# Kernel optimization log

Measured on AMD Instinct MI355X. Metric: run time of the kernel, lower is better.

The kernel has to match this reference:

```python
import jax, jax.numpy as jnp
import numpy as np
from jax import lax

MIN_VALUE = 0.0
MAX_VALUE = 1.0

# 5-point Laplacian stencil kernel, OIHW layout
_LAP_KERNEL = jnp.array([[0.0, 1.0, 0.0],
                         [1.0, -4.0, 1.0],
                         [0.0, 1.0, 0.0]], dtype=jnp.float32).reshape(1, 1, 3, 3)


def _laplacian(u):
    # u: [B, 1, H, W], zero-padded 3x3 stencil (SAME)
    return lax.conv_general_dilated(
        u, _LAP_KERNEL, window_strides=(1, 1), padding='SAME',
        dimension_numbers=('NCHW', 'OIHW', 'NCHW'))


def _step(u, params):
    # Fisher-Kolmogorov reaction-diffusion step:
    #   diff = D * laplacian(u) + rho * u * (1 - u)
    D = params[:, 0:1]    # [B,1,H,W]
    rho = params[:, 1:2]  # [B,1,H,W]
    return D * _laplacian(u) + rho * u * (1.0 - u)


def setup_inputs() -> dict:
    key = jax.random.key(0)
    k1, k2, k3 = jax.random.split(key, 3)
    B, H, W = 32, 256, 256
    u = jax.random.uniform(k1, (B, 1, H, W), dtype=jnp.float32)
    params = jax.random.uniform(k2, (B, 2, H, W), dtype=jnp.float32)
    t = jax.random.randint(k3, (B,), 0, 32, dtype=jnp.int32)
    return {"u": u, "params": params, "t": t}


def reference(u, params, t):
    # Original: for step in range(max(t)): u[t>step] += step(u[t>step], params[t>step]); clip(u).
    # The step is per-sample local, so masked gather/scatter == predicated full update.
    max_duration = int(jnp.max(t))  # static trip count

    def body(step, u):
        mask = (t > step).astype(u.dtype)[:, None, None, None]  # [B,1,1,1]
        u = u + mask * _step(u, params)
        return jnp.clip(u, MIN_VALUE, MAX_VALUE)

    return lax.fori_loop(0, max_duration, body, u)
```

## Files before the change

### kernel.cpp

```cpp
#include <hip/hip_runtime.h>

#define HH 256
#define WW 256
#define PLANE (HH * WW)
#define CORE 32
#define HALO 8
#define SLAB 48
#define NW 16
#define RPW 3

__global__ __launch_bounds__(1024, 4)
void rd_group_kernel(const float* __restrict__ uin,
                     const float* __restrict__ params,
                     const int* __restrict__ t,
                     float* __restrict__ uout,
                     int base, int k)
{
    __shared__ float4 vt[NW][64];
    __shared__ float4 vb[NW][64];

    const int blk   = blockIdx.x;
    const int b     = blk >> 3;
    const int strip = blk & 7;
    const int r0    = strip * CORE;
    const int w     = threadIdx.x >> 6;
    const int lane  = threadIdx.x & 63;
    const int c0    = lane << 2;

    const int growbase = r0 - HALO + RPW * w;

    int ls = t[b] - base;
    ls = ls < 0 ? 0 : (ls > k ? k : ls);

    float u[RPW][4], pD[RPW][4], pR[RPW][4];
    bool inimg[RPW];

    const size_t ubase = (size_t)b * PLANE;
    const size_t pbase = (size_t)b * 2 * PLANE;

    #pragma unroll
    for (int dr = 0; dr < RPW; ++dr) {
        const int grow = growbase + dr;
        inimg[dr] = (grow >= 0) && (grow < HH);
        if (inimg[dr]) {
            const float4 uu = *reinterpret_cast<const float4*>(uin + ubase + (size_t)grow * WW + c0);
            const float4 dd = *reinterpret_cast<const float4*>(params + pbase + (size_t)grow * WW + c0);
            const float4 rr = *reinterpret_cast<const float4*>(params + pbase + PLANE + (size_t)grow * WW + c0);
            u[dr][0] = uu.x; u[dr][1] = uu.y; u[dr][2] = uu.z; u[dr][3] = uu.w;
            pD[dr][0] = dd.x; pD[dr][1] = dd.y; pD[dr][2] = dd.z; pD[dr][3] = dd.w;
            pR[dr][0] = rr.x; pR[dr][1] = rr.y; pR[dr][2] = rr.z; pR[dr][3] = rr.w;
        } else {
            #pragma unroll
            for (int c = 0; c < 4; ++c) { u[dr][c] = 0.f; pD[dr][c] = 0.f; pR[dr][c] = 0.f; }
        }
    }

    for (int s = 0; s < ls; ++s) {
        vt[w][lane] = make_float4(u[0][0], u[0][1], u[0][2], u[0][3]);
        vb[w][lane] = make_float4(u[RPW-1][0], u[RPW-1][1], u[RPW-1][2], u[RPW-1][3]);
        __syncthreads();

        float upr[4] = {0.f, 0.f, 0.f, 0.f};
        float dnr[4] = {0.f, 0.f, 0.f, 0.f};
        if (w > 0)      { float4 v = vb[w-1][lane]; upr[0]=v.x; upr[1]=v.y; upr[2]=v.z; upr[3]=v.w; }
        if (w < NW - 1) { float4 v = vt[w+1][lane]; dnr[0]=v.x; dnr[1]=v.y; dnr[2]=v.z; dnr[3]=v.w; }

        float nu[RPW][4];
        #pragma unroll
        for (int dr = 0; dr < RPW; ++dr) {
            float lf = __shfl_up(u[dr][3], 1);
            if (lane == 0)  lf = 0.f;
            float rt = __shfl_down(u[dr][0], 1);
            if (lane == 63) rt = 0.f;

            #pragma unroll
            for (int c = 0; c < 4; ++c) {
                const float upv = dr ? u[dr-1][c] : upr[c];
                const float dnv = (dr < RPW - 1) ? u[dr+1][c] : dnr[c];
                const float lv  = c ? u[dr][c-1] : lf;
                const float rv  = (c < 3) ? u[dr][c+1] : rt;
                const float uc  = u[dr][c];
                const float lap = upv + dnv + lv + rv - 4.0f * uc;
                float un = uc + pD[dr][c] * lap + pR[dr][c] * (uc * (1.0f - uc));
                un = fminf(fmaxf(un, 0.0f), 1.0f);
                nu[dr][c] = un;
            }
        }
        #pragma unroll
        for (int dr = 0; dr < RPW; ++dr) {
            #pragma unroll
            for (int c = 0; c < 4; ++c)
                u[dr][c] = inimg[dr] ? nu[dr][c] : 0.f;
        }
        __syncthreads();
    }

    #pragma unroll
    for (int dr = 0; dr < RPW; ++dr) {
        const int grow = growbase + dr;
        if (grow >= r0 && grow < r0 + CORE) {
            *reinterpret_cast<float4*>(uout + ubase + (size_t)grow * WW + c0) =
                make_float4(u[dr][0], u[dr][1], u[dr][2], u[dr][3]);
        }
    }
}

extern "C" void kernel_launch(void* const* d_in, const int* in_sizes, int n_in,
                              void* d_out, int out_size, void* d_ws, size_t ws_size,
                              hipStream_t stream) {
    (void)in_sizes; (void)n_in; (void)out_size; (void)ws_size;
    const float* u      = (const float*)d_in[0];
    const float* params = (const float*)d_in[1];
    const int*   t      = (const int*)d_in[2];
    float*       out    = (float*)d_out;
    float*       ws     = (float*)d_ws;

    const dim3 grid(256), block(1024);
    rd_group_kernel<<<grid, block, 0, stream>>>(u,   params, t, ws,  0,  8);
    rd_group_kernel<<<grid, block, 0, stream>>>(ws,  params, t, out, 8,  8);
    rd_group_kernel<<<grid, block, 0, stream>>>(out, params, t, ws,  16, 8);
    rd_group_kernel<<<grid, block, 0, stream>>>(ws,  params, t, out, 24, 7);
}
```

Measured before the change: 60.06 us.

## Deepen temporal blocking to 16 steps per launch with double-buffered halo exchange

Widens the halo from 8 to 16 rows with 4 rows per wave, which halves the number of launches from four to two. Each launch therefore re-reads u and params from global memory half as often. Shared-memory halo buffers are now double-buffered, which removes one __syncthreads per step. Rows that cannot influence the core within the remaining steps skip their loads, and the per-step clamp to zero outside the image is dropped in favour of zero params. The cost is more redundant halo compute (64 rows computed per 32 stored) and more registers per thread.

```diff
diff --git a/kernel.cpp b/kernel.cpp
--- a/kernel.cpp
+++ b/kernel.cpp
@@ -4,20 +4,20 @@
 #define WW 256
 #define PLANE (HH * WW)
 #define CORE 32
-#define HALO 8
-#define SLAB 48
+#define HALO 16
+#define SLAB 64
 #define NW 16
-#define RPW 3
+#define RPW 4
 
 __global__ __launch_bounds__(1024, 4)
-void rd_group_kernel(const float* __restrict__ uin,
-                     const float* __restrict__ params,
-                     const int* __restrict__ t,
-                     float* __restrict__ uout,
-                     int base, int k)
+void rd_tb16_kernel(const float* __restrict__ uin,
+                    const float* __restrict__ params,
+                    const int* __restrict__ t,
+                    float* __restrict__ uout,
+                    int base, int k)
 {
-    __shared__ float4 vt[NW][64];
-    __shared__ float4 vb[NW][64];
+    __shared__ float4 vt[2][NW][64];
+    __shared__ float4 vb[2][NW][64];
 
     const int blk   = blockIdx.x;
     const int b     = blk >> 3;
@@ -27,78 +27,91 @@
     const int lane  = threadIdx.x & 63;
     const int c0    = lane << 2;
 
-    const int growbase = r0 - HALO + RPW * w;
-
     int ls = t[b] - base;
     ls = ls < 0 ? 0 : (ls > k ? k : ls);
 
-    float u[RPW][4], pD[RPW][4], pR[RPW][4];
-    bool inimg[RPW];
-
+    const int growbase = r0 - HALO + RPW * w;
     const size_t ubase = (size_t)b * PLANE;
     const size_t pbase = (size_t)b * 2 * PLANE;
+
+    float u[RPW][4], pD[RPW][4], pR[RPW][4];
 
     #pragma unroll
     for (int dr = 0; dr < RPW; ++dr) {
         const int grow = growbase + dr;
-        inimg[dr] = (grow >= 0) && (grow < HH);
-        if (inimg[dr]) {
+        const bool inimg = (grow >= 0) && (grow < HH);
+        int dist = 0;
+        if (grow < r0)             dist = r0 - grow;
+        else if (grow > r0 + CORE - 1) dist = grow - (r0 + CORE - 1);
+        const bool needU = inimg && (dist <= ls);
+        const bool needP = inimg && (dist < ls);
+
+        if (needU) {
             const float4 uu = *reinterpret_cast<const float4*>(uin + ubase + (size_t)grow * WW + c0);
+            u[dr][0] = uu.x; u[dr][1] = uu.y; u[dr][2] = uu.z; u[dr][3] = uu.w;
+        } else {
+            u[dr][0] = u[dr][1] = u[dr][2] = u[dr][3] = 0.f;
+        }
+        if (needP) {
             const float4 dd = *reinterpret_cast<const float4*>(params + pbase + (size_t)grow * WW + c0);
             const float4 rr = *reinterpret_cast<const float4*>(params + pbase + PLANE + (size_t)grow * WW + c0);
-            u[dr][0] = uu.x; u[dr][1] = uu.y; u[dr][2] = uu.z; u[dr][3] = uu.w;
             pD[dr][0] = dd.x; pD[dr][1] = dd.y; pD[dr][2] = dd.z; pD[dr][3] = dd.w;
             pR[dr][0] = rr.x; pR[dr][1] = rr.y; pR[dr][2] = rr.z; pR[dr][3] = rr.w;
         } else {
-            #pragma unroll
-            for (int c = 0; c < 4; ++c) { u[dr][c] = 0.f; pD[dr][c] = 0.f; pR[dr][c] = 0.f; }
+            pD[dr][0] = pD[dr][1] = pD[dr][2] = pD[dr][3] = 0.f;
+            pR[dr][0] = pR[dr][1] = pR[dr][2] = pR[dr][3] = 0.f;
         }
     }
 
-    for (int s = 0; s < ls; ++s) {
-        vt[w][lane] = make_float4(u[0][0], u[0][1], u[0][2], u[0][3]);
-        vb[w][lane] = make_float4(u[RPW-1][0], u[RPW-1][1], u[RPW-1][2], u[RPW-1][3]);
-        __syncthreads();
+    if (ls > 0) {
+        vt[0][w][lane] = make_float4(u[0][0], u[0][1], u[0][2], u[0][3]);
+        vb[0][w][lane] = make_float4(u[RPW-1][0], u[RPW-1][1], u[RPW-1][2], u[RPW-1][3]);
 
-        float upr[4] = {0.f, 0.f, 0.f, 0.f};
-        float dnr[4] = {0.f, 0.f, 0.f, 0.f};
-        if (w > 0)      { float4 v = vb[w-1][lane]; upr[0]=v.x; upr[1]=v.y; upr[2]=v.z; upr[3]=v.w; }
-        if (w < NW - 1) { float4 v = vt[w+1][lane]; dnr[0]=v.x; dnr[1]=v.y; dnr[2]=v.z; dnr[3]=v.w; }
+        for (int s = 0; s < ls; ++s) {
+            __syncthreads();
+            const int cur = s & 1;
 
-        float nu[RPW][4];
+            float upr[4] = {0.f, 0.f, 0.f, 0.f};
+            float dnr[4] = {0.f, 0.f, 0.f, 0.f};
+            if (w > 0)      { float4 v = vb[cur][w-1][lane]; upr[0]=v.x; upr[1]=v.y; upr[2]=v.z; upr[3]=v.w; }
+            if (w < NW - 1) { float4 v = vt[cur][w+1][lane]; dnr[0]=v.x; dnr[1]=v.y; dnr[2]=v.z; dnr[3]=v.w; }
+
+            float nu[RPW][4];
+            #pragma unroll
+            for (int dr = 0; dr < RPW; ++dr) {
+                float lf = __shfl_up(u[dr][3], 1);
+                if (lane == 0)  lf = 0.f;
+                float rt = __shfl_down(u[dr][0], 1);
+                if (lane == 63) rt = 0.f;
+
+                #pragma unroll
+                for (int c = 0; c < 4; ++c) {
+                    const float upv = dr ? u[dr-1][c] : upr[c];
+                    const float dnv = (dr < RPW - 1) ? u[dr+1][c] : dnr[c];
+                    const float lv  = c ? u[dr][c-1] : lf;
+                    const float rv  = (c < 3) ? u[dr][c+1] : rt;
+                    const float uc  = u[dr][c];
+                    const float lap = upv + dnv + lv + rv - 4.0f * uc;
+                    float un = uc + pD[dr][c] * lap + pR[dr][c] * (uc * (1.0f - uc));
+                    nu[dr][c] = fminf(fmaxf(un, 0.0f), 1.0f);
+                }
+            }
+            #pragma unroll
+            for (int dr = 0; dr < RPW; ++dr)
+                #pragma unroll
+                for (int c = 0; c < 4; ++c)
+                    u[dr][c] = nu[dr][c];
+
+            const int nxt = cur ^ 1;
+            vt[nxt][w][lane] = make_float4(u[0][0], u[0][1], u[0][2], u[0][3]);
+            vb[nxt][w][lane] = make_float4(u[RPW-1][0], u[RPW-1][1], u[RPW-1][2], u[RPW-1][3]);
+        }
+    }
+
+    if (w >= HALO / RPW && w < (HALO + CORE) / RPW) {
         #pragma unroll
         for (int dr = 0; dr < RPW; ++dr) {
-            float lf = __shfl_up(u[dr][3], 1);
-            if (lane == 0)  lf = 0.f;
-            float rt = __shfl_down(u[dr][0], 1);
-            if (lane == 63) rt = 0.f;
-
-            #pragma unroll
-            for (int c = 0; c < 4; ++c) {
-                const float upv = dr ? u[dr-1][c] : upr[c];
-                const float dnv = (dr < RPW - 1) ? u[dr+1][c] : dnr[c];
-                const float lv  = c ? u[dr][c-1] : lf;
-                const float rv  = (c < 3) ? u[dr][c+1] : rt;
-                const float uc  = u[dr][c];
-                const float lap = upv + dnv + lv + rv - 4.0f * uc;
-                float un = uc + pD[dr][c] * lap + pR[dr][c] * (uc * (1.0f - uc));
-                un = fminf(fmaxf(un, 0.0f), 1.0f);
-                nu[dr][c] = un;
-            }
-        }
-        #pragma unroll
-        for (int dr = 0; dr < RPW; ++dr) {
-            #pragma unroll
-            for (int c = 0; c < 4; ++c)
-                u[dr][c] = inimg[dr] ? nu[dr][c] : 0.f;
-        }
-        __syncthreads();
-    }
-
-    #pragma unroll
-    for (int dr = 0; dr < RPW; ++dr) {
-        const int grow = growbase + dr;
-        if (grow >= r0 && grow < r0 + CORE) {
+            const int grow = growbase + dr;
             *reinterpret_cast<float4*>(uout + ubase + (size_t)grow * WW + c0) =
                 make_float4(u[dr][0], u[dr][1], u[dr][2], u[dr][3]);
         }
@@ -116,8 +129,6 @@
     float*       ws     = (float*)d_ws;
 
     const dim3 grid(256), block(1024);
-    rd_group_kernel<<<grid, block, 0, stream>>>(u,   params, t, ws,  0,  8);
-    rd_group_kernel<<<grid, block, 0, stream>>>(ws,  params, t, out, 8,  8);
-    rd_group_kernel<<<grid, block, 0, stream>>>(out, params, t, ws,  16, 8);
-    rd_group_kernel<<<grid, block, 0, stream>>>(ws,  params, t, out, 24, 7);
+    rd_tb16_kernel<<<grid, block, 0, stream>>>(u,  params, t, ws,  0,  16);
+    rd_tb16_kernel<<<grid, block, 0, stream>>>(ws, params, t, out, 16, 15);
 }
```

After: 51.63 us. 1.16x faster.
